# Kernel tuning notes

Hardware: AMD Instinct MI355X
Metric: run time of the kernel (lower is better)

Reference implementation:

```python
import jax, jax.numpy as jnp
import numpy as np

N = 100000

def _gcn_conv(x, W, b, row, col, norm, n_nodes):
    # x: [N, Fin], W: [Fin, Fout]; message = norm * (x W)[row], aggregated at col
    h = x @ W                                  # small GEMM
    msg = h[row] * norm[:, None]               # [E+N, Fout] gather (memory bound)
    out = jax.ops.segment_sum(msg, col, num_segments=n_nodes)
    return out + b

def _norm_coeffs(edge_index, n_nodes):
    # add self-loops, compute symmetric normalization deg^-1/2[row]*deg^-1/2[col]
    loops = jnp.arange(n_nodes, dtype=edge_index.dtype)
    row = jnp.concatenate([edge_index[0], loops])
    col = jnp.concatenate([edge_index[1], loops])
    deg = jax.ops.segment_sum(jnp.ones_like(col, dtype=jnp.float32), col,
                              num_segments=n_nodes)
    dinv = jnp.where(deg > 0, jax.lax.rsqrt(deg), 0.0)
    norm = dinv[row] * dinv[col]
    return row, col, norm

def setup_inputs() -> dict:
    key = jax.random.key(0)
    ks = jax.random.split(key, 4)
    x = jax.random.normal(ks[0], (N, 64), dtype=jnp.float32)
    edge_index = jax.random.randint(ks[1], (2, 1600000), 0, N, dtype=jnp.int64)
    W1 = jax.random.normal(ks[2], (64, 64), dtype=jnp.float32) / np.sqrt(64)
    b1 = jnp.zeros((64,), dtype=jnp.float32)
    W2 = jax.random.normal(ks[3], (64, 64), dtype=jnp.float32) / np.sqrt(64)
    b2 = jnp.zeros((64,), dtype=jnp.float32)
    return {"x": x, "edge_index": edge_index, "W1": W1, "b1": b1, "W2": W2, "b2": b2}

def reference(x, edge_index, W1, b1, W2, b2):
    row, col, norm = _norm_coeffs(edge_index, N)
    h = jax.nn.relu(_gcn_conv(x, W1, b1, row, col, norm, N))
    return _gcn_conv(h, W2, b2, row, col, norm, N)
```

## Files before the change

### kernel.cpp

```cpp
#include <hip/hip_runtime.h>


#define NPB 32
#define BSH 8
#define BSZ 256
#define PTILE 4096
#define CAP 6144
#define PADALLOW 3856
#define CROW (CAP + PADALLOW)

typedef __attribute__((ext_vector_type(8))) short bf16x8;
typedef __attribute__((ext_vector_type(4))) float f32x4;

__device__ __forceinline__ unsigned bf16_rne(float f) {
    unsigned b = __float_as_uint(f);
    return (b + 0x7fffu + ((b >> 16) & 1u)) >> 16;
}
__device__ __forceinline__ float bf16_lo(unsigned u) { return __uint_as_float(u << 16); }
__device__ __forceinline__ float bf16_hi(unsigned u) { return __uint_as_float(u & 0xffff0000u); }

__global__ __launch_bounds__(512) void k_count(const int* __restrict__ coli,
                                               int E, int N, int NB, int numTiles,
                                               int* __restrict__ tcnt) {
    __shared__ int hist[512];
    int t = threadIdx.x;
    int T = E + N;
    int tile = blockIdx.x;
    int tstart = tile * PTILE;
    int m = min(PTILE, T - tstart);
    for (int b = t; b < NB; b += 512) hist[b] = 0;
    __syncthreads();
    for (int i = t; i < m; i += 512) {
        int g = tstart + i;
        int c = (g < E) ? coli[g] : (g - E);
        atomicAdd(&hist[c >> BSH], 1);
    }
    __syncthreads();
    for (int b = t; b < NB; b += 512) tcnt[(size_t)tile * NB + b] = hist[b];
}

__global__ __launch_bounds__(512) void k_scan(int* __restrict__ tcnt,
                                              int* __restrict__ btot,
                                              int NB, int numTiles) {
    __shared__ int wsum[8];
    int b = blockIdx.x;
    int t = threadIdx.x;
    int lane = t & 63, wid = t >> 6;
    int base = 0;
    for (int c0 = 0; c0 < numTiles; c0 += 512) {
        int tt = c0 + t;
        int v = (tt < numTiles) ? tcnt[(size_t)tt * NB + b] : 0;
        int inc = v;
        #pragma unroll
        for (int d = 1; d < 64; d <<= 1) {
            int o = __shfl_up(inc, d);
            if (lane >= d) inc += o;
        }
        if (lane == 63) wsum[wid] = inc;
        __syncthreads();
        int woff = 0, ctot = 0;
        #pragma unroll
        for (int i = 0; i < 8; i++) {
            int s = wsum[i];
            if (i < wid) woff += s;
            ctot += s;
        }
        if (tt < numTiles) tcnt[(size_t)tt * NB + b] = b * CAP + base + woff + inc - v;
        base += ctot;
        __syncthreads();
    }
    if (t == 0) btot[b] = base;
}

__global__ __launch_bounds__(512) void k_scatter(const int* __restrict__ rowi,
                                                 const int* __restrict__ coli,
                                                 int E, int N, int NB, int numTiles,
                                                 const int* __restrict__ tcnt,
                                                 unsigned* __restrict__ pairs) {
    __shared__ int scur[512];
    int t = threadIdx.x;
    int T = E + N;
    int tile = blockIdx.x;
    int tstart = tile * PTILE;
    int m = min(PTILE, T - tstart);
    for (int b = t; b < NB; b += 512) scur[b] = tcnt[(size_t)tile * NB + b];
    __syncthreads();
    for (int i = t; i < m; i += 512) {
        int g = tstart + i;
        int r, c;
        if (g < E) { r = rowi[g]; c = coli[g]; }
        else       { r = g - E; c = r; }
        int b = c >> BSH;
        int slot = atomicAdd(&scur[b], 1);
        pairs[slot] = (unsigned)r | ((unsigned)(c & (BSZ - 1)) << 24);
    }
}

__global__ __launch_bounds__(1024) void k_bfill(const unsigned* __restrict__ pairs,
                                                const int* __restrict__ btot,
                                                int N,
                                                int* __restrict__ offsets,
                                                int* __restrict__ cnt,
                                                float* __restrict__ dinv,
                                                int* __restrict__ csrc) {
    __shared__ int scnt[BSZ];
    __shared__ int scur[BSZ];
    __shared__ int wsum[4];
    int b = blockIdx.x;
    int t = threadIdx.x;
    int ebeg = b * CAP;
    int m = btot[b];
    int pbase = b * CROW;
    if (t < BSZ) scnt[t] = 0;
    __syncthreads();
    for (int i = t; i < m; i += 1024) {
        atomicAdd(&scnt[pairs[ebeg + i] >> 24], 1);
    }
    __syncthreads();
    int cval = 0, pc = 0, inc = 0;
    int lane = t & 63, wid = t >> 6;
    if (t < BSZ) {
        cval = scnt[t];
        pc = (cval + 15) & ~15;
        inc = pc;
        #pragma unroll
        for (int d = 1; d < 64; d <<= 1) {
            int o = __shfl_up(inc, d);
            if (lane >= d) inc += o;
        }
        if (lane == 63) wsum[wid] = inc;
    }
    __syncthreads();
    if (t < BSZ) {
        int woff = 0;
        for (int i = 0; i < wid; i++) woff += wsum[i];
        int off = pbase + woff + inc - pc;
        int v = (b << BSH) + t;
        if (v < N) {
            offsets[v] = off;
            cnt[v] = (cval + 1) & ~1;
            dinv[v] = rsqrtf((float)cval);
        }
        scur[t] = off;
        for (int i = off + cval; i < off + pc; i++) csrc[i] = N;
    }
    __syncthreads();
    for (int i = t; i < m; i += 1024) {
        unsigned pk = pairs[ebeg + i];
        int slot = atomicAdd(&scur[pk >> 24], 1);
        csrc[slot] = (int)(pk & 0xFFFFFFu);
    }
}

template <bool BF16IN>
__global__ __launch_bounds__(256) void k_gemm(const void* __restrict__ Xv,
                                              const float* __restrict__ W,
                                              const float* __restrict__ dinv,
                                              unsigned* __restrict__ Hout,
                                              int N, int nSlabs, int slabStride) {
    __shared__ float SMEM[4224];
    int t = threadIdx.x;
    int lane = t & 63, w = t >> 6;
    int nn = lane & 15, kq = lane >> 4;

    for (int i = t; i < 1024; i += 256) ((float4*)SMEM)[i] = ((const float4*)W)[i];
    __syncthreads();
    bf16x8 Bf[2][4];
    #pragma unroll
    for (int kt = 0; kt < 2; kt++) {
        #pragma unroll
        for (int ct = 0; ct < 4; ct++) {
            union { bf16x8 v; unsigned short s[8]; } u;
            #pragma unroll
            for (int j = 0; j < 8; j++) {
                int k = kt * 32 + kq * 8 + j;
                u.s[j] = (unsigned short)bf16_rne(SMEM[k * 64 + ct * 16 + nn]);
            }
            Bf[kt][ct] = u.v;
        }
    }
    __syncthreads();

    float* outT = SMEM + w * 1056;

    for (int slab = blockIdx.x * 4 + w; slab < nSlabs; slab += slabStride) {
        int row0 = slab * 16;
        int rowA = min(row0 + nn, N - 1);
        bf16x8 A0, A1;
        if (BF16IN) {
            const uint4* X = (const uint4*)Xv;
            union { uint4 u; bf16x8 v; } a0, a1;
            a0.u = X[(size_t)rowA * 8 + kq];
            a1.u = X[(size_t)rowA * 8 + 4 + kq];
            A0 = a0.v; A1 = a1.v;
        } else {
            const float4* X = (const float4*)Xv;
            float4 f0 = X[(size_t)rowA * 16 + kq * 2];
            float4 f1 = X[(size_t)rowA * 16 + kq * 2 + 1];
            float4 f2 = X[(size_t)rowA * 16 + 8 + kq * 2];
            float4 f3 = X[(size_t)rowA * 16 + 8 + kq * 2 + 1];
            union { bf16x8 v; unsigned short s[8]; } a0, a1;
            a0.s[0] = (unsigned short)bf16_rne(f0.x); a0.s[1] = (unsigned short)bf16_rne(f0.y);
            a0.s[2] = (unsigned short)bf16_rne(f0.z); a0.s[3] = (unsigned short)bf16_rne(f0.w);
            a0.s[4] = (unsigned short)bf16_rne(f1.x); a0.s[5] = (unsigned short)bf16_rne(f1.y);
            a0.s[6] = (unsigned short)bf16_rne(f1.z); a0.s[7] = (unsigned short)bf16_rne(f1.w);
            a1.s[0] = (unsigned short)bf16_rne(f2.x); a1.s[1] = (unsigned short)bf16_rne(f2.y);
            a1.s[2] = (unsigned short)bf16_rne(f2.z); a1.s[3] = (unsigned short)bf16_rne(f2.w);
            a1.s[4] = (unsigned short)bf16_rne(f3.x); a1.s[5] = (unsigned short)bf16_rne(f3.y);
            a1.s[6] = (unsigned short)bf16_rne(f3.z); a1.s[7] = (unsigned short)bf16_rne(f3.w);
            A0 = a0.v; A1 = a1.v;
        }
        float dvm = dinv[rowA];

        f32x4 acc[4];
        #pragma unroll
        for (int ct = 0; ct < 4; ct++) acc[ct] = (f32x4){0.f, 0.f, 0.f, 0.f};
        #pragma unroll
        for (int ct = 0; ct < 4; ct++) {
            acc[ct] = __builtin_amdgcn_mfma_f32_16x16x32_bf16(A0, Bf[0][ct], acc[ct], 0, 0, 0);
            acc[ct] = __builtin_amdgcn_mfma_f32_16x16x32_bf16(A1, Bf[1][ct], acc[ct], 0, 0, 0);
        }

        #pragma unroll
        for (int reg = 0; reg < 4; reg++) {
            int r = kq * 4 + reg;
            float dv = __shfl(dvm, r);
            #pragma unroll
            for (int ct = 0; ct < 4; ct++) {
                outT[r * 66 + ct * 16 + nn] = acc[ct][reg] * dv;
            }
        }
        int rr = lane >> 2;
        int c0 = (lane & 3) * 16;
        int orow = row0 + rr;
        if (orow < N) {
            unsigned pk[8];
            #pragma unroll
            for (int i = 0; i < 8; i++) {
                float lo = outT[rr * 66 + c0 + 2 * i];
                float hi = outT[rr * 66 + c0 + 2 * i + 1];
                pk[i] = bf16_rne(lo) | (bf16_rne(hi) << 16);
            }
            uint4* dst = (uint4*)Hout + (size_t)orow * 8 + (lane & 3) * 2;
            dst[0] = make_uint4(pk[0], pk[1], pk[2], pk[3]);
            dst[1] = make_uint4(pk[4], pk[5], pk[6], pk[7]);
        } else if (orow == N) {
            uint4* dst = (uint4*)Hout + (size_t)N * 8 + (lane & 3) * 2;
            dst[0] = make_uint4(0, 0, 0, 0);
            dst[1] = make_uint4(0, 0, 0, 0);
        }
    }
}

template <bool RELU_BF16OUT>
__global__ __launch_bounds__(256) void k_agg(const uint4* __restrict__ H,
                                             const int* __restrict__ offsets,
                                             const int* __restrict__ cnt,
                                             const int* __restrict__ csrc,
                                             const float* __restrict__ dinv,
                                             const float* __restrict__ bias,
                                             void* __restrict__ outv, int N) {
    int t = threadIdx.x;
    int fl = t & 7;
    int v = blockIdx.x * NPB + (t >> 3);
    if (v >= N) return;
    int beg = offsets[v];
    int deg = cnt[v];
    const int2* cs2 = (const int2*)(csrc + beg);
    const char* hb = (const char*)H + ((unsigned)fl << 4);

    float a0 = 0.f, a1 = 0.f, a2 = 0.f, a3 = 0.f;
    float a4 = 0.f, a5 = 0.f, a6 = 0.f, a7 = 0.f;

#define ACC8(R) do {                                                        \
        uint4 dd = *(const uint4*)(hb + ((unsigned)(R) << 7));              \
        a0 += bf16_lo(dd.x); a1 += bf16_hi(dd.x);                           \
        a2 += bf16_lo(dd.y); a3 += bf16_hi(dd.y);                           \
        a4 += bf16_lo(dd.z); a5 += bf16_hi(dd.z);                           \
        a6 += bf16_lo(dd.w); a7 += bf16_hi(dd.w);                           \
    } while (0)

    int2 ss = cs2[0];
    for (int j = 2; j < deg; j += 2) {
        int2 nx = cs2[j >> 1];
        ACC8(ss.x);
        ACC8(ss.y);
        ss = nx;
    }
    ACC8(ss.x);
    ACC8(ss.y);
#undef ACC8

    float dv = dinv[v];
    const float4* b4 = (const float4*)bias;
    float4 bA = b4[fl * 2];
    float4 bB = b4[fl * 2 + 1];
    float r0 = fmaf(dv, a0, bA.x);
    float r1 = fmaf(dv, a1, bA.y);
    float r2 = fmaf(dv, a2, bA.z);
    float r3 = fmaf(dv, a3, bA.w);
    float r4 = fmaf(dv, a4, bB.x);
    float r5 = fmaf(dv, a5, bB.y);
    float r6 = fmaf(dv, a6, bB.z);
    float r7 = fmaf(dv, a7, bB.w);
    if (RELU_BF16OUT) {
        r0 = fmaxf(r0, 0.f); r1 = fmaxf(r1, 0.f);
        r2 = fmaxf(r2, 0.f); r3 = fmaxf(r3, 0.f);
        r4 = fmaxf(r4, 0.f); r5 = fmaxf(r5, 0.f);
        r6 = fmaxf(r6, 0.f); r7 = fmaxf(r7, 0.f);
        uint4 pk;
        pk.x = bf16_rne(r0) | (bf16_rne(r1) << 16);
        pk.y = bf16_rne(r2) | (bf16_rne(r3) << 16);
        pk.z = bf16_rne(r4) | (bf16_rne(r5) << 16);
        pk.w = bf16_rne(r6) | (bf16_rne(r7) << 16);
        ((uint4*)outv)[(size_t)v * 8 + fl] = pk;
    } else {
        float4* o = (float4*)outv + (size_t)v * 16 + fl * 2;
        o[0] = make_float4(r0, r1, r2, r3);
        o[1] = make_float4(r4, r5, r6, r7);
    }
}

extern "C" void kernel_launch(void* const* d_in, const int* in_sizes, int n_in,
                              void* d_out, int out_size, void* d_ws, size_t ws_size,
                              hipStream_t stream) {
    const float* x  = (const float*)d_in[0];
    const int*   ei = (const int*)d_in[1];
    const float* W1 = (const float*)d_in[2];
    const float* b1 = (const float*)d_in[3];
    const float* W2 = (const float*)d_in[4];
    const float* b2 = (const float*)d_in[5];
    float* out      = (float*)d_out;

    const int N = in_sizes[0] / 64;
    const int E = in_sizes[1] / 2;
    const int* row = ei;
    const int* col = ei + E;
    const int T = E + N;
    const int NB = (N + BSZ - 1) >> BSH;
    const int numTiles = (T + PTILE - 1) / PTILE;

    char* p = (char*)d_ws;
    auto alloc = [&](size_t bytes) { void* r = (void*)p; p += (bytes + 255) & ~(size_t)255; return r; };
    int*      tcnt    = (int*)alloc((size_t)NB * numTiles * 4);
    int*      btot    = (int*)alloc((size_t)(NB + 1) * 4);
    int*      offsets = (int*)alloc((size_t)N * 4);
    int*      cnt     = (int*)alloc((size_t)N * 4);
    float*    dinv    = (float*)alloc((size_t)N * 4);
    unsigned* pairs   = (unsigned*)alloc((size_t)NB * CAP * 4);
    int*      csrc    = (int*)alloc(((size_t)NB * CROW + 64) * 4);
    unsigned* hbuf    = (unsigned*)alloc((size_t)(N + 16) * 32 * 4);
    unsigned* abuf    = (unsigned*)alloc((size_t)(N + 16) * 32 * 4);

    k_count<<<numTiles, 512, 0, stream>>>(col, E, N, NB, numTiles, tcnt);
    k_scan<<<NB, 512, 0, stream>>>(tcnt, btot, NB, numTiles);
    k_scatter<<<numTiles, 512, 0, stream>>>(row, col, E, N, NB, numTiles, tcnt, pairs);
    k_bfill<<<NB, 1024, 0, stream>>>(pairs, btot, N, offsets, cnt, dinv, csrc);

    const int nSlabs = (N + 16) / 16;
    const int GEMM_BLOCKS = 1024;
    const int SLAB_STRIDE = GEMM_BLOCKS * 4;
    const int GB = (N + NPB - 1) / NPB;

    k_gemm<false><<<GEMM_BLOCKS, 256, 0, stream>>>(x, W1, dinv, hbuf, N, nSlabs, SLAB_STRIDE);
    k_agg<true><<<GB, 256, 0, stream>>>((const uint4*)hbuf, offsets, cnt, csrc, dinv, b1, abuf, N);
    k_gemm<true><<<GEMM_BLOCKS, 256, 0, stream>>>(abuf, W2, dinv, hbuf, N, nSlabs, SLAB_STRIDE);
    k_agg<false><<<GB, 256, 0, stream>>>((const uint4*)hbuf, offsets, cnt, csrc, dinv, b2, out, N);
}
```

Before: 204.1 us.

## Stage bucket scatter and CSR fill in shared memory for coalesced writes

The scatter kernel now builds a local histogram per tile, computes bucket offsets with a block scan, sorts pairs into shared memory, then writes them to global memory in bucket-contiguous runs instead of issuing random global writes. The bfill kernel likewise builds the per-bucket CSR source list in shared memory and copies it out contiguously. This targets uncoalesced scattered global stores, at the cost of extra LDS use (roughly 30KB and 40KB per block), extra passes and barriers, and possibly lower occupancy.

After: 198.0 us. 3.0% less time.

```diff
diff --git a/kernel.cpp b/kernel.cpp
--- a/kernel.cpp
+++ b/kernel.cpp
@@ -77,22 +77,71 @@
                                                  int E, int N, int NB, int numTiles,
                                                  const int* __restrict__ tcnt,
                                                  unsigned* __restrict__ pairs) {
-    __shared__ int scur[512];
+    __shared__ int hist[512];
+    __shared__ int lbase[512];
+    __shared__ int gbase[512];
+    __shared__ unsigned sorted[PTILE];
+    __shared__ unsigned short sbkt[PTILE];
+    __shared__ int wsum[8];
     int t = threadIdx.x;
     int T = E + N;
     int tile = blockIdx.x;
     int tstart = tile * PTILE;
     int m = min(PTILE, T - tstart);
-    for (int b = t; b < NB; b += 512) scur[b] = tcnt[(size_t)tile * NB + b];
-    __syncthreads();
-    for (int i = t; i < m; i += 512) {
-        int g = tstart + i;
-        int r, c;
-        if (g < E) { r = rowi[g]; c = coli[g]; }
-        else       { r = g - E; c = r; }
-        int b = c >> BSH;
-        int slot = atomicAdd(&scur[b], 1);
-        pairs[slot] = (unsigned)r | ((unsigned)(c & (BSZ - 1)) << 24);
+    for (int b = t; b < NB; b += 512) {
+        hist[b] = 0;
+        gbase[b] = tcnt[(size_t)tile * NB + b];
+    }
+    __syncthreads();
+    int c_reg[8];
+    #pragma unroll
+    for (int k = 0; k < 8; k++) {
+        int i = t + k * 512;
+        int c = 0;
+        if (i < m) {
+            int g = tstart + i;
+            c = (g < E) ? coli[g] : (g - E);
+            atomicAdd(&hist[c >> BSH], 1);
+        }
+        c_reg[k] = c;
+    }
+    __syncthreads();
+    {
+        int lane = t & 63, wid = t >> 6;
+        int v = (t < NB) ? hist[t] : 0;
+        int inc = v;
+        #pragma unroll
+        for (int d = 1; d < 64; d <<= 1) {
+            int o = __shfl_up(inc, d);
+            if (lane >= d) inc += o;
+        }
+        if (lane == 63) wsum[wid] = inc;
+        __syncthreads();
+        int woff = 0;
+        for (int i = 0; i < wid; i++) woff += wsum[i];
+        if (t < NB) lbase[t] = woff + inc - v;
+        __syncthreads();
+    }
+    for (int b = t; b < NB; b += 512) hist[b] = 0;
+    __syncthreads();
+    #pragma unroll
+    for (int k = 0; k < 8; k++) {
+        int i = t + k * 512;
+        if (i < m) {
+            int g = tstart + i;
+            int c = c_reg[k];
+            int r = (g < E) ? rowi[g] : c;
+            int b = c >> BSH;
+            int lr = atomicAdd(&hist[b], 1);
+            int pos = lbase[b] + lr;
+            sorted[pos] = (unsigned)r | ((unsigned)(c & (BSZ - 1)) << 24);
+            sbkt[pos] = (unsigned short)b;
+        }
+    }
+    __syncthreads();
+    for (int j = t; j < m; j += 512) {
+        int b = sbkt[j];
+        pairs[gbase[b] + (j - lbase[b])] = sorted[j];
     }
 }
 
@@ -106,6 +155,7 @@
     __shared__ int scnt[BSZ];
     __shared__ int scur[BSZ];
     __shared__ int wsum[4];
+    __shared__ int scsrc[CROW];
     int b = blockIdx.x;
     int t = threadIdx.x;
     int ebeg = b * CAP;
@@ -134,22 +184,25 @@
     if (t < BSZ) {
         int woff = 0;
         for (int i = 0; i < wid; i++) woff += wsum[i];
-        int off = pbase + woff + inc - pc;
+        int offl = woff + inc - pc;
         int v = (b << BSH) + t;
         if (v < N) {
-            offsets[v] = off;
+            offsets[v] = pbase + offl;
             cnt[v] = (cval + 1) & ~1;
             dinv[v] = rsqrtf((float)cval);
         }
-        scur[t] = off;
-        for (int i = off + cval; i < off + pc; i++) csrc[i] = N;
+        scur[t] = offl;
+        for (int i = offl + cval; i < offl + pc; i++) scsrc[i] = N;
     }
     __syncthreads();
     for (int i = t; i < m; i += 1024) {
         unsigned pk = pairs[ebeg + i];
         int slot = atomicAdd(&scur[pk >> 24], 1);
-        csrc[slot] = (int)(pk & 0xFFFFFFu);
-    }
+        scsrc[slot] = (int)(pk & 0xFFFFFFu);
+    }
+    __syncthreads();
+    int tot = wsum[0] + wsum[1] + wsum[2] + wsum[3];
+    for (int j = t; j < tot; j += 1024) csrc[pbase + j] = scsrc[j];
 }
 
 template <bool BF16IN>
```
